# Kernel tuning notes

Hardware: AMD Instinct MI355X
Metric: run time of the kernel (lower is better)

## Reference

```python
import jax, jax.numpy as jnp
import numpy as np

N = 50000          # nodes
E = 1600000        # edges (avg degree 32)
G = 16             # graphs in batch
H = 128            # hidden_dim
HOP = 3
IN_DIM = 1


def setup_inputs() -> dict:
    key = jax.random.key(0)
    ks = jax.random.split(key, 12)
    s = 1.0 / np.sqrt(H)
    return {
        "x": jax.random.normal(ks[0], (N, IN_DIM), jnp.float32),
        "edge_index": jax.random.randint(ks[1], (2, E), 0, N, jnp.int64),
        "edge_attr": jax.random.uniform(ks[2], (E, 1), jnp.float32),
        "batch": jnp.sort(jax.random.randint(ks[3], (N,), 0, G, jnp.int64)),
        "W1": jax.random.normal(ks[4], (HOP, H, IN_DIM), jnp.float32) * s,
        "W2": jax.random.normal(ks[5], (HOP, H, H), jnp.float32) * s,
        "W3": jax.random.normal(ks[6], (HOP, H, H), jnp.float32) * s,
        "W4": jax.random.normal(ks[7], (HOP, H, 1), jnp.float32) * s,
        "W5": jax.random.normal(ks[8], (1, 2 * H), jnp.float32) * s,
        "b5": jnp.zeros((1,), jnp.float32),
        "W6": jax.random.normal(ks[9], (H, H), jnp.float32) * s,
        "W7": jax.random.normal(ks[10], (H, H), jnp.float32) * s,
    }


def reference(x, edge_index, edge_attr, batch, W1, W2, W3, W4, W5, b5, W6, W7):
    row, col = edge_index[0], edge_index[1]
    node_emb = jnp.zeros((N, H), x.dtype)
    for l in range(HOP):
        nfe = x @ W1[l].T                                        # [N,H]
        # gather neighbor embeddings along col, scatter-add to row
        ne_aggr = jax.ops.segment_sum(node_emb[col], row, num_segments=N)
        efe = jax.nn.relu(edge_attr @ W4[l].T)                   # [E,H]
        ee_aggr = jax.ops.segment_sum(efe, row, num_segments=N)  # [N,H]
        node_emb = jax.nn.relu(nfe + ne_aggr @ W2[l].T + ee_aggr @ W3[l].T)
    pooled = jax.ops.segment_sum(node_emb, batch, num_segments=G)  # [G,H]
    sum_emb = pooled @ W6.T                                        # [G,H]
    cat = jax.nn.relu(jnp.concatenate([sum_emb[batch], node_emb @ W7.T], axis=-1))
    return cat @ W5.T + b5                                         # [N,1]
```

## Files before the change

### kernel.cpp

```cpp
#include <hip/hip_runtime.h>
#include <hip/hip_bf16.h>

#define N_NODES 50000
#define N_EDGES 1600000
#define NGRAPH  16
#define HID     128

#define RPB   128
#define NB    ((N_NODES + RPB - 1) / RPB)
#define NBLK  256
#define EPB   ((N_EDGES + NBLK - 1) / NBLK)

typedef unsigned int uint32;
typedef unsigned short ushort;
typedef unsigned char uchar;
typedef __attribute__((ext_vector_type(8))) short bf16x8;
typedef __attribute__((ext_vector_type(4))) float f32x4;
typedef __attribute__((ext_vector_type(2))) float f32x2;

__device__ __forceinline__ uint32 bf16r(float f) {
    uint32 b = __float_as_uint(f);
    return (b + 0x7fffu + ((b >> 16) & 1u)) >> 16;
}
__device__ __forceinline__ uint32 pack_bf16(float lo, float hi) {
    return bf16r(lo) | (bf16r(hi) << 16);
}
__device__ __forceinline__ float bf_lo(uint32 u) { return __uint_as_float(u << 16); }
__device__ __forceinline__ float bf_hi(uint32 u) { return __uint_as_float(u & 0xffff0000u); }

__global__ __launch_bounds__(256) void k_init(float* p, int n,
                                              const int* __restrict__ batch,
                                              int* __restrict__ gstart) {
    int i = blockIdx.x * 256 + threadIdx.x;
    if (i < n) p[i] = 0.f;
    if (i <= NGRAPH) {
        int lo = 0, hi = N_NODES;
        while (lo < hi) {
            int mid = (lo + hi) >> 1;
            if (batch[mid] < i) lo = mid + 1; else hi = mid;
        }
        gstart[i] = lo;
    }
}

__global__ __launch_bounds__(1024) void k_p1_hist(const int* __restrict__ row,
                                                  int* __restrict__ blkhist) {
    __shared__ int hist[NB];
    int tid = threadIdx.x, blk = blockIdx.x;
    for (int i = tid; i < NB; i += 1024) hist[i] = 0;
    __syncthreads();
    int s = blk * EPB, e = s + EPB; if (e > N_EDGES) e = N_EDGES;
    for (int i = s + tid; i < e; i += 1024)
        atomicAdd(&hist[row[i] >> 7], 1);
    __syncthreads();
    for (int i = tid; i < NB; i += 1024)
        blkhist[i * NBLK + blk] = hist[i];
}

__global__ __launch_bounds__(NBLK) void k_p2a(int* __restrict__ blkhist,
                                              int* __restrict__ btot) {
    __shared__ int sums[NBLK];
    int t = threadIdx.x, b = blockIdx.x;
    int v = blkhist[b * NBLK + t];
    sums[t] = v;
    __syncthreads();
    for (int d = 1; d < NBLK; d <<= 1) {
        int u = (t >= d) ? sums[t - d] : 0;
        __syncthreads();
        sums[t] += u;
        __syncthreads();
    }
    blkhist[b * NBLK + t] = sums[t] - v;
    if (t == NBLK - 1) btot[b] = sums[t];
}

__global__ __launch_bounds__(512) void k_p2b(const int* __restrict__ btot,
                                             int* __restrict__ bbase) {
    __shared__ int sums[512];
    int t = threadIdx.x;
    int s = (t < NB) ? btot[t] : 0;
    sums[t] = s;
    __syncthreads();
    for (int d = 1; d < 512; d <<= 1) {
        int v = (t >= d) ? sums[t - d] : 0;
        __syncthreads();
        sums[t] += v;
        __syncthreads();
    }
    if (t < NB) {
        bbase[t] = sums[t] - s;
        if (t == NB - 1) bbase[NB] = sums[t];
    }
}

__global__ __launch_bounds__(1024) void k_p3_part(const int* __restrict__ row,
                                                  const int* __restrict__ col,
                                                  const float* __restrict__ ea,
                                                  const int* __restrict__ blkhist,
                                                  const int* __restrict__ bbase,
                                                  int2* __restrict__ pea) {
    __shared__ int cur[NB];
    int tid = threadIdx.x, blk = blockIdx.x;
    for (int i = tid; i < NB; i += 1024)
        cur[i] = bbase[i] + blkhist[i * NBLK + blk];
    __syncthreads();
    int s = blk * EPB, e = s + EPB; if (e > N_EDGES) e = N_EDGES;
    for (int i = s + tid; i < e; i += 1024) {
        int r = row[i], c = col[i];
        float a = ea[i];
        int slot = atomicAdd(&cur[r >> 7], 1);
        pea[slot] = make_int2(((r & (RPB - 1)) << 16) | c, __float_as_int(a));
    }
}

__global__ __launch_bounds__(512) void k_p4a(const int2* __restrict__ pea,
                                             const int* __restrict__ bbase,
                                             const float* __restrict__ x,
                                             int* __restrict__ offs,
                                             float* __restrict__ ea_sum,
                                             float2* __restrict__ pxe) {
    __shared__ int   cnt[RPB];
    __shared__ float eas[RPB];
    __shared__ int   scan_s[RPB];
    int tid = threadIdx.x, b = blockIdx.x;
    if (tid < RPB) { cnt[tid] = 0; eas[tid] = 0.f; }
    __syncthreads();
    int s = bbase[b], e = bbase[b + 1];
    for (int i = s + tid; i < e; i += 512) {
        int2 p = pea[i];
        int lr = ((uint32)p.x) >> 16;
        atomicAdd(&cnt[lr], 1);
        atomicAdd(&eas[lr], __int_as_float(p.y));
    }
    __syncthreads();
    if (tid < RPB) scan_s[tid] = cnt[tid];
    __syncthreads();
    for (int d = 1; d < RPB; d <<= 1) {
        int v = 0;
        if (tid < RPB && tid >= d) v = scan_s[tid - d];
        __syncthreads();
        if (tid < RPB) scan_s[tid] += v;
        __syncthreads();
    }
    int nbase = b * RPB;
    if (tid < RPB) {
        int excl = scan_s[tid] - cnt[tid];
        int n = nbase + tid;
        if (n < N_NODES) {
            offs[n] = s + excl;
            ea_sum[n] = eas[tid];
            pxe[n] = make_float2(x[n], eas[tid]);
        }
    }
    if (b == NB - 1 && tid == 0) offs[N_NODES] = e;
}

__global__ __launch_bounds__(512) void k_p4b(const int2* __restrict__ pea,
                                             const int* __restrict__ bbase,
                                             const int* __restrict__ offs,
                                             const float2* __restrict__ pxe,
                                             int* __restrict__ csr,
                                             float2* __restrict__ pxec) {
    __shared__ int cur[RPB];
    int tid = threadIdx.x, b = blockIdx.x;
    int nbase = b * RPB;
    if (tid < RPB) cur[tid] = (nbase + tid < N_NODES) ? offs[nbase + tid] : 0;
    __syncthreads();
    int s = bbase[b], e = bbase[b + 1];
    for (int i = s + tid; i < e; i += 512) {
        int2 p = pea[i];
        int c = p.x & 0xFFFF;
        int slot = atomicAdd(&cur[((uint32)p.x) >> 16], 1);
        csr[slot] = c;
        pxec[slot] = pxe[c];
    }
}

__global__ __launch_bounds__(256) void k_prep(const float* __restrict__ W2,
                                              const float* __restrict__ W7,
                                              const float* __restrict__ W3,
                                              const float* __restrict__ W4,
                                              ushort* __restrict__ wpack,
                                              float* __restrict__ v3) {
    int idx = blockIdx.x * 256 + threadIdx.x;
    if (idx < 4 * 16384) {
        int m = idx >> 14, f = idx & 16383;
        int j = f & 7, lane = (f >> 3) & 63, kk = (f >> 9) & 3, t = (f >> 11) & 7;
        int hp = t * 16 + (lane & 15);
        int k  = kk * 32 + ((lane >> 4) & 3) * 8 + j;
        const float* src = (m < 3) ? (W2 + m * HID * HID) : W7;
        wpack[idx] = (ushort)bf16r(src[hp * HID + k]);
    }
    if (idx < 3 * HID) {
        int l = idx / HID, hp = idx % HID;
        float acc = 0.f;
        for (int h = 0; h < HID; h++)
            acc += W3[l * HID * HID + hp * HID + h] * fmaxf(W4[l * HID + h], 0.f);
        v3[idx] = acc;
    }
}

__global__ __launch_bounds__(256) void k_gather1(const float2* __restrict__ pxec,
                                                 const int* __restrict__ offs,
                                                 const float* __restrict__ w1,
                                                 const float* __restrict__ v3,
                                                 uint32* __restrict__ agg) {
    int node = (blockIdx.x * 256 + threadIdx.x) >> 6;
    int lane = threadIdx.x & 63;
    if (node >= N_NODES) return;
    f32x2 w1v = {w1[2 * lane], w1[2 * lane + 1]};
    f32x2 v3v = {v3[2 * lane], v3[2 * lane + 1]};
    const f32x2 zero = {0.f, 0.f};
    int s = offs[node], e = offs[node + 1];
    f32x2 acc[4] = {zero, zero, zero, zero};
    int j = s;
    for (; j + 8 <= e; j += 8) {
        float2 p[8];
#pragma unroll
        for (int u = 0; u < 8; u++) p[u] = pxec[j + u];
#pragma unroll
        for (int u = 0; u < 8; u++) {
            f32x2 px = {p[u].x, p[u].x};
            f32x2 pe = {p[u].y, p[u].y};
            f32x2 r = __builtin_elementwise_fma(px, w1v, pe * v3v);
            acc[u & 3] += __builtin_elementwise_max(r, zero);
        }
    }
    for (; j < e; j++) {
        float2 p = pxec[j];
        f32x2 px = {p.x, p.x};
        f32x2 pe = {p.y, p.y};
        f32x2 r = __builtin_elementwise_fma(px, w1v, pe * v3v);
        acc[0] += __builtin_elementwise_max(r, zero);
    }
    f32x2 rs = (acc[0] + acc[1]) + (acc[2] + acc[3]);
    agg[(size_t)node * 64 + lane] = pack_bf16(rs.x, rs.y);
}

__global__ __launch_bounds__(256) void k_gather(const uchar* __restrict__ emb8,
                                                const int* __restrict__ offs,
                                                const int* __restrict__ csr,
                                                uint32* __restrict__ agg) {
    int node = (blockIdx.x * 256 + threadIdx.x) >> 6;
    int lane = threadIdx.x & 63;
    if (node >= N_NODES) return;
    int s = offs[node], e = offs[node + 1];
    float ax[8] = {0.f}, ay[8] = {0.f};
    for (int base = s; base < e; base += 64) {
        int idx = base + lane;
        int cv = (idx < e) ? csr[idx] : 0;
        int cnt = e - base; if (cnt > 64) cnt = 64;
        int j = 0;
        for (; j + 8 <= cnt; j += 8) {
            int h16[8];
#pragma unroll
            for (int u = 0; u < 8; u++) {
                int c = __shfl(cv, j + u);
                h16[u] = *(const ushort*)(emb8 + (size_t)c * 128 + 2 * lane);
            }
#pragma unroll
            for (int u = 0; u < 8; u++) {
                f32x2 d = __builtin_amdgcn_cvt_pk_f32_fp8(h16[u], false);
                ax[u] += d.x; ay[u] += d.y;
            }
        }
        for (; j < cnt; j++) {
            int c = __shfl(cv, j);
            int h = *(const ushort*)(emb8 + (size_t)c * 128 + 2 * lane);
            f32x2 d = __builtin_amdgcn_cvt_pk_f32_fp8(h, false);
            ax[0] += d.x; ay[0] += d.y;
        }
    }
    float rx = (((ax[0] + ax[1]) + (ax[2] + ax[3])) + ((ax[4] + ax[5]) + (ax[6] + ax[7]))) * 64.f;
    float ry = (((ay[0] + ay[1]) + (ay[2] + ay[3])) + ((ay[4] + ay[5]) + (ay[6] + ay[7]))) * 64.f;
    agg[(size_t)node * 64 + lane] = pack_bf16(rx, ry);
}

#define LROW 136

template <bool LAST>
__global__ __launch_bounds__(256) void k_gemm(const uint32* __restrict__ agg,
                                              const ushort* __restrict__ w2p,
                                              const float* __restrict__ w1l,
                                              const float* __restrict__ v3l,
                                              const float* __restrict__ x,
                                              const float* __restrict__ ea_sum,
                                              uint32* __restrict__ embOut,
                                              uchar* __restrict__ emb8Out,
                                              const ushort* __restrict__ w7p,
                                              const float* __restrict__ W5,
                                              float* __restrict__ outp) {
    __shared__ ushort tile[64 * LROW];
    int tid = threadIdx.x;
    int tbase = blockIdx.x * 64;
    {
        const uint2* src = (const uint2*)(agg + (size_t)tbase * 64);
        int vn = N_NODES - tbase; if (vn > 64) vn = 64;
        int lim = vn * 32;
        for (int i = tid; i < 64 * 32; i += 256) {
            uint2 u = (i < lim) ? src[i] : make_uint2(0u, 0u);
            int r = i >> 5, c4 = (i & 31) * 4;
            *(uint2*)&tile[r * LROW + c4] = u;
        }
    }
    __syncthreads();
    int wv = tid >> 6, lane = tid & 63;
    int n0 = lane & 15, quad = lane >> 4;
    int arow = wv * 16 + n0;
    bf16x8 a0 = *(const bf16x8*)&tile[arow * LROW + 0 * 32 + quad * 8];
    bf16x8 a1 = *(const bf16x8*)&tile[arow * LROW + 1 * 32 + quad * 8];
    bf16x8 a2 = *(const bf16x8*)&tile[arow * LROW + 2 * 32 + quad * 8];
    bf16x8 a3 = *(const bf16x8*)&tile[arow * LROW + 3 * 32 + quad * 8];
    const bf16x8* wb = (const bf16x8*)w2p;
    f32x4 acc[8];
#pragma unroll
    for (int t = 0; t < 8; t++) {
        f32x4 c = {0.f, 0.f, 0.f, 0.f};
        c = __builtin_amdgcn_mfma_f32_16x16x32_bf16(a0, wb[(t * 4 + 0) * 64 + lane], c, 0, 0, 0);
        c = __builtin_amdgcn_mfma_f32_16x16x32_bf16(a1, wb[(t * 4 + 1) * 64 + lane], c, 0, 0, 0);
        c = __builtin_amdgcn_mfma_f32_16x16x32_bf16(a2, wb[(t * 4 + 2) * 64 + lane], c, 0, 0, 0);
        c = __builtin_amdgcn_mfma_f32_16x16x32_bf16(a3, wb[(t * 4 + 3) * 64 + lane], c, 0, 0, 0);
        acc[t] = c;
    }
    float xs[4], es[4];
#pragma unroll
    for (int r = 0; r < 4; r++) {
        int n = tbase + wv * 16 + quad * 4 + r;
        xs[r] = (n < N_NODES) ? x[n] : 0.f;
        es[r] = (n < N_NODES) ? ea_sum[n] : 0.f;
    }
    if (!LAST) {
        uchar* stile = (uchar*)tile;
#pragma unroll
        for (int t = 0; t < 8; t++) {
            int hp = t * 16 + n0;
            float w1v = w1l[hp], v3v = v3l[hp];
#pragma unroll
            for (int r = 0; r < 4; r++) {
                float v = fmaxf(acc[t][r] + xs[r] * w1v + es[r] * v3v, 0.f) * 0.015625f;
                int enc = __builtin_amdgcn_cvt_pk_fp8_f32(v, v, 0, false);
                stile[(wv * 16 + quad * 4 + r) * 136 + hp] = (uchar)(enc & 0xff);
            }
        }
        __syncthreads();
        int vn = N_NODES - tbase; if (vn > 64) vn = 64;
        for (int i = tid; i < 64 * 32; i += 256) {
            int r = i >> 5, c4 = (i & 31) * 4;
            if (r < vn) {
                uint32 u = *(const uint32*)&stile[r * 136 + c4];
                *(uint32*)(emb8Out + (size_t)(tbase + r) * 128 + c4) = u;
            }
        }
    } else {
#pragma unroll
        for (int t = 0; t < 8; t++) {
            int hp = t * 16 + n0;
            float w1v = w1l[hp], v3v = v3l[hp];
#pragma unroll
            for (int r = 0; r < 4; r++) {
                float v = fmaxf(acc[t][r] + xs[r] * w1v + es[r] * v3v, 0.f);
                tile[(wv * 16 + quad * 4 + r) * LROW + hp] = (ushort)bf16r(v);
            }
        }
        __syncthreads();
        {
            int vn = N_NODES - tbase; if (vn > 64) vn = 64;
            for (int i = tid; i < 64 * 32; i += 256) {
                int r = i >> 5, c4 = (i & 31) * 4;
                if (r < vn) {
                    uint2 u = *(const uint2*)&tile[r * LROW + c4];
                    *(uint2*)(embOut + (size_t)(tbase + r) * 64 + (size_t)(i & 31) * 2) = u;
                }
            }
        }
        bf16x8 b0 = *(const bf16x8*)&tile[arow * LROW + 0 * 32 + quad * 8];
        bf16x8 b1 = *(const bf16x8*)&tile[arow * LROW + 1 * 32 + quad * 8];
        bf16x8 b2 = *(const bf16x8*)&tile[arow * LROW + 2 * 32 + quad * 8];
        bf16x8 b3 = *(const bf16x8*)&tile[arow * LROW + 3 * 32 + quad * 8];
        const bf16x8* w7 = (const bf16x8*)w7p;
        float p[4] = {0.f, 0.f, 0.f, 0.f};
#pragma unroll
        for (int t = 0; t < 8; t++) {
            f32x4 c = {0.f, 0.f, 0.f, 0.f};
            c = __builtin_amdgcn_mfma_f32_16x16x32_bf16(b0, w7[(t * 4 + 0) * 64 + lane], c, 0, 0, 0);
            c = __builtin_amdgcn_mfma_f32_16x16x32_bf16(b1, w7[(t * 4 + 1) * 64 + lane], c, 0, 0, 0);
            c = __builtin_amdgcn_mfma_f32_16x16x32_bf16(b2, w7[(t * 4 + 2) * 64 + lane], c, 0, 0, 0);
            c = __builtin_amdgcn_mfma_f32_16x16x32_bf16(b3, w7[(t * 4 + 3) * 64 + lane], c, 0, 0, 0);
            float w5v = W5[128 + t * 16 + n0];
#pragma unroll
            for (int r = 0; r < 4; r++) p[r] += fmaxf(c[r], 0.f) * w5v;
        }
#pragma unroll
        for (int r = 0; r < 4; r++) {
            float v = p[r];
            v += __shfl_xor(v, 1);
            v += __shfl_xor(v, 2);
            v += __shfl_xor(v, 4);
            v += __shfl_xor(v, 8);
            int n = tbase + wv * 16 + quad * 4 + r;
            if (n0 == 0 && n < N_NODES) outp[n] = v;
        }
    }
}

__global__ __launch_bounds__(256) void k_pool2(const uint32* __restrict__ emb,
                                               const int* __restrict__ gstart,
                                               float* __restrict__ pooled) {
    __shared__ float2 red[4][64];
    int bid = blockIdx.x;
    int g = bid >> 4, chunk = bid & 15;
    int gs = gstart[g], ge = gstart[g + 1];
    int len = ge - gs;
    int cs = gs + (int)(((long long)len * chunk) >> 4);
    int ce = gs + (int)(((long long)len * (chunk + 1)) >> 4);
    int sub = threadIdx.x >> 6, lane = threadIdx.x & 63;
    float ax = 0.f, ay = 0.f;
    for (int n = cs + sub; n < ce; n += 4) {
        uint32 u = emb[(size_t)n * 64 + lane];
        ax += bf_lo(u); ay += bf_hi(u);
    }
    red[sub][lane] = make_float2(ax, ay);
    __syncthreads();
    if (sub == 0) {
        float2 r0 = red[0][lane], r1 = red[1][lane], r2 = red[2][lane], r3 = red[3][lane];
        atomicAdd(&pooled[g * HID + 2 * lane],     (r0.x + r1.x) + (r2.x + r3.x));
        atomicAdd(&pooled[g * HID + 2 * lane + 1], (r0.y + r1.y) + (r2.y + r3.y));
    }
}

__global__ __launch_bounds__(128) void k_graph(const float* __restrict__ pooled,
                                               const float* __restrict__ W6,
                                               const float* __restrict__ W5,
                                               float* __restrict__ s_g) {
    int g = blockIdx.x, hp = threadIdx.x;
    float acc = 0.f;
    for (int h = 0; h < HID; h++) acc += pooled[g * HID + h] * W6[hp * HID + h];
    float v = fmaxf(acc, 0.f) * W5[hp];
    __shared__ float red[HID];
    red[hp] = v;
    __syncthreads();
    for (int d = 64; d > 0; d >>= 1) {
        if (hp < d) red[hp] += red[hp + d];
        __syncthreads();
    }
    if (hp == 0) s_g[g] = red[0];
}

__global__ __launch_bounds__(256) void k_addsg(float* __restrict__ out,
                                               const int* __restrict__ batch,
                                               const float* __restrict__ s_g,
                                               const float* __restrict__ b5) {
    int n = blockIdx.x * 256 + threadIdx.x;
    if (n < N_NODES) out[n] += s_g[batch[n]] + b5[0];
}

extern "C" void kernel_launch(void* const* d_in, const int* in_sizes, int n_in,
                              void* d_out, int out_size, void* d_ws, size_t ws_size,
                              hipStream_t stream) {
    (void)in_sizes; (void)n_in; (void)out_size; (void)ws_size;
    const float* x    = (const float*)d_in[0];
    const int*   ei   = (const int*)d_in[1];
    const float* ea   = (const float*)d_in[2];
    const int*   bat  = (const int*)d_in[3];
    const float* W1   = (const float*)d_in[4];
    const float* W2   = (const float*)d_in[5];
    const float* W3   = (const float*)d_in[6];
    const float* W4   = (const float*)d_in[7];
    const float* W5   = (const float*)d_in[8];
    const float* b5   = (const float*)d_in[9];
    const float* W6   = (const float*)d_in[10];
    const float* W7   = (const float*)d_in[11];
    float* out = (float*)d_out;

    const int* row = ei;
    const int* col = ei + N_EDGES;

    float* wsf = (float*)d_ws;
    int*   wsi = (int*)d_ws;
    size_t o = 0;
    float* pooled = wsf + o; o += NGRAPH * HID;
    float* s_g    = wsf + o; o += NGRAPH;
    size_t ztot = o;
    int*   offs   = wsi + o; o += N_NODES + 1;
    float* ea_sum = wsf + o; o += N_NODES;
    int*   gstart = wsi + o; o += NGRAPH + 1;
    int*   btot   = wsi + o; o += NB;
    int*   bbase  = wsi + o; o += NB + 1;
    float* v3     = wsf + o; o += 3 * HID;
    int*   blkh   = wsi + o; o += NB * NBLK;
    o = (o + 1) & ~(size_t)1;
    float2* pxe   = (float2*)(wsi + o); o += 2 * (size_t)N_NODES;
    o = (o + 3) & ~(size_t)3;
    ushort* wpack = (ushort*)(wsi + o); o += 4 * 16384 / 2;
    int*    csr   = wsi + o; o += N_EDGES;
    o = (o + 1) & ~(size_t)1;
    int2*   pea   = (int2*)(wsi + o); o += 2 * (size_t)N_EDGES;
    float2* pxec  = (float2*)(wsi + o); o += 2 * (size_t)N_EDGES;
    o = (o + 1) & ~(size_t)1;
    uint32* embA  = (uint32*)(wsi + o); o += (size_t)N_NODES * 64;
    uchar*  emb8  = (uchar*)(wsi + o);  o += (size_t)N_NODES * 32;
    uint32* aggB  = (uint32*)(wsi + o); o += (size_t)N_NODES * 64;

    const ushort* w2p1 = wpack + 1 * 16384;
    const ushort* w2p2 = wpack + 2 * 16384;
    const ushort* w7p  = wpack + 3 * 16384;

    k_init<<<(int)((ztot + 255) / 256), 256, 0, stream>>>((float*)d_ws, (int)ztot, bat, gstart);
    k_p1_hist<<<NBLK, 1024, 0, stream>>>(row, blkh);
    k_p2a<<<NB, NBLK, 0, stream>>>(blkh, btot);
    k_p2b<<<1, 512, 0, stream>>>(btot, bbase);
    k_p3_part<<<NBLK, 1024, 0, stream>>>(row, col, ea, blkh, bbase, pea);
    k_p4a<<<NB, 512, 0, stream>>>(pea, bbase, x, offs, ea_sum, pxe);
    k_p4b<<<NB, 512, 0, stream>>>(pea, bbase, offs, pxe, csr, pxec);
    k_prep<<<(4 * 16384 + 255) / 256, 256, 0, stream>>>(W2, W7, W3, W4, (ushort*)wpack, v3);
    k_gather1<<<(N_NODES * 64 + 255) / 256, 256, 0, stream>>>(pxec, offs, W1, v3, aggB);
    k_gemm<false><<<(N_NODES + 63) / 64, 256, 0, stream>>>(
        aggB, w2p1, W1 + 1 * HID, v3 + 1 * HID, x, ea_sum, nullptr, emb8, nullptr, nullptr, nullptr);
    k_gather<<<(N_NODES * 64 + 255) / 256, 256, 0, stream>>>(emb8, offs, csr, aggB);
    k_gemm<true><<<(N_NODES + 63) / 64, 256, 0, stream>>>(
        aggB, w2p2, W1 + 2 * HID, v3 + 2 * HID, x, ea_sum, embA, nullptr, w7p, W5, out);
    k_pool2<<<NGRAPH * 16, 256, 0, stream>>>(embA, gstart, pooled);
    k_graph<<<NGRAPH, 128, 0, stream>>>(pooled, W6, W5, s_g);
    k_addsg<<<(N_NODES + 255) / 256, 256, 0, stream>>>(out, bat, s_g, b5);
}
```

Before: 283.5 us.

## Split fp8 embeddings into feature planes and fuse small kernels via last-block pattern

The fp8 node embedding is stored as two 64-byte feature planes. The layer-2 gather now runs twice as many blocks, one per plane, with each lane reading a single byte, which shrinks the per-plane working set so it fits better in cache during random neighbour gathers. Weight packing moves into the init kernel. The two scan kernels and the pool/graph kernels are each merged using an atomic done-counter so the last block finishes the work. This removes several launches but adds atomics, threadfence and serial tail work in a single block.

```diff
diff --git a/kernel.cpp b/kernel.cpp
--- a/kernel.cpp
+++ b/kernel.cpp
@@ -10,6 +10,8 @@
 #define NB    ((N_NODES + RPB - 1) / RPB)
 #define NBLK  256
 #define EPB   ((N_EDGES + NBLK - 1) / NBLK)
+#define PLANESZ ((size_t)N_NODES * 64)
+#define GBLK  ((N_NODES * 64) / 256)
 
 typedef unsigned int uint32;
 typedef unsigned short ushort;
@@ -28,18 +30,39 @@
 __device__ __forceinline__ float bf_lo(uint32 u) { return __uint_as_float(u << 16); }
 __device__ __forceinline__ float bf_hi(uint32 u) { return __uint_as_float(u & 0xffff0000u); }
 
-__global__ __launch_bounds__(256) void k_init(float* p, int n,
+__global__ __launch_bounds__(256) void k_init(float* __restrict__ zp, int zn,
                                               const int* __restrict__ batch,
-                                              int* __restrict__ gstart) {
-    int i = blockIdx.x * 256 + threadIdx.x;
-    if (i < n) p[i] = 0.f;
-    if (i <= NGRAPH) {
+                                              int* __restrict__ gstart,
+                                              const float* __restrict__ W2,
+                                              const float* __restrict__ W7,
+                                              const float* __restrict__ W3,
+                                              const float* __restrict__ W4,
+                                              ushort* __restrict__ wpack,
+                                              float* __restrict__ v3) {
+    int idx = blockIdx.x * 256 + threadIdx.x;
+    if (idx < zn) zp[idx] = 0.f;
+    if (idx <= NGRAPH) {
         int lo = 0, hi = N_NODES;
         while (lo < hi) {
             int mid = (lo + hi) >> 1;
-            if (batch[mid] < i) lo = mid + 1; else hi = mid;
-        }
-        gstart[i] = lo;
+            if (batch[mid] < idx) lo = mid + 1; else hi = mid;
+        }
+        gstart[idx] = lo;
+    }
+    if (idx < 4 * 16384) {
+        int m = idx >> 14, f = idx & 16383;
+        int j = f & 7, lane = (f >> 3) & 63, kk = (f >> 9) & 3, t = (f >> 11) & 7;
+        int hp = t * 16 + (lane & 15);
+        int k  = kk * 32 + ((lane >> 4) & 3) * 8 + j;
+        const float* src = (m < 3) ? (W2 + m * HID * HID) : W7;
+        wpack[idx] = (ushort)bf16r(src[hp * HID + k]);
+    }
+    if (idx < 3 * HID) {
+        int l = idx / HID, hp = idx % HID;
+        float acc = 0.f;
+        for (int h = 0; h < HID; h++)
+            acc += W3[l * HID * HID + hp * HID + h] * fmaxf(W4[l * HID + h], 0.f);
+        v3[idx] = acc;
     }
 }
 
@@ -57,9 +80,12 @@
         blkhist[i * NBLK + blk] = hist[i];
 }
 
-__global__ __launch_bounds__(NBLK) void k_p2a(int* __restrict__ blkhist,
-                                              int* __restrict__ btot) {
+__global__ __launch_bounds__(NBLK) void k_p2(int* __restrict__ blkhist,
+                                             int* __restrict__ btot,
+                                             int* __restrict__ bbase,
+                                             int* __restrict__ done) {
     __shared__ int sums[NBLK];
+    __shared__ int lastflag;
     int t = threadIdx.x, b = blockIdx.x;
     int v = blkhist[b * NBLK + t];
     sums[t] = v;
@@ -72,24 +98,29 @@
     }
     blkhist[b * NBLK + t] = sums[t] - v;
     if (t == NBLK - 1) btot[b] = sums[t];
-}
-
-__global__ __launch_bounds__(512) void k_p2b(const int* __restrict__ btot,
-                                             int* __restrict__ bbase) {
-    __shared__ int sums[512];
-    int t = threadIdx.x;
-    int s = (t < NB) ? btot[t] : 0;
-    sums[t] = s;
-    __syncthreads();
-    for (int d = 1; d < 512; d <<= 1) {
-        int v = (t >= d) ? sums[t - d] : 0;
-        __syncthreads();
-        sums[t] += v;
-        __syncthreads();
-    }
-    if (t < NB) {
-        bbase[t] = sums[t] - s;
-        if (t == NB - 1) bbase[NB] = sums[t];
+    if (t == 0) {
+        __threadfence();
+        int old = atomicAdd(done, 1);
+        lastflag = (old == NB - 1);
+    }
+    __syncthreads();
+    if (lastflag) {
+        int i0 = 2 * t, i1 = 2 * t + 1;
+        int v0 = (i0 < NB) ? atomicAdd(&btot[i0], 0) : 0;
+        int v1 = (i1 < NB) ? atomicAdd(&btot[i1], 0) : 0;
+        int sum = v0 + v1;
+        sums[t] = sum;
+        __syncthreads();
+        for (int d = 1; d < NBLK; d <<= 1) {
+            int u = (t >= d) ? sums[t - d] : 0;
+            __syncthreads();
+            sums[t] += u;
+            __syncthreads();
+        }
+        int excl = sums[t] - sum;
+        if (i0 < NB) bbase[i0] = excl;
+        if (i1 < NB) bbase[i1] = excl + v0;
+        if (t == NBLK - 1) bbase[NB] = sums[t];
     }
 }
 
@@ -173,30 +204,6 @@
         int slot = atomicAdd(&cur[((uint32)p.x) >> 16], 1);
         csr[slot] = c;
         pxec[slot] = pxe[c];
-    }
-}
-
-__global__ __launch_bounds__(256) void k_prep(const float* __restrict__ W2,
-                                              const float* __restrict__ W7,
-                                              const float* __restrict__ W3,
-                                              const float* __restrict__ W4,
-                                              ushort* __restrict__ wpack,
-                                              float* __restrict__ v3) {
-    int idx = blockIdx.x * 256 + threadIdx.x;
-    if (idx < 4 * 16384) {
-        int m = idx >> 14, f = idx & 16383;
-        int j = f & 7, lane = (f >> 3) & 63, kk = (f >> 9) & 3, t = (f >> 11) & 7;
-        int hp = t * 16 + (lane & 15);
-        int k  = kk * 32 + ((lane >> 4) & 3) * 8 + j;
-        const float* src = (m < 3) ? (W2 + m * HID * HID) : W7;
-        wpack[idx] = (ushort)bf16r(src[hp * HID + k]);
-    }
-    if (idx < 3 * HID) {
-        int l = idx / HID, hp = idx % HID;
-        float acc = 0.f;
-        for (int h = 0; h < HID; h++)
-            acc += W3[l * HID * HID + hp * HID + h] * fmaxf(W4[l * HID + h], 0.f);
-        v3[idx] = acc;
     }
 }
 
@@ -237,43 +244,45 @@
     agg[(size_t)node * 64 + lane] = pack_bf16(rs.x, rs.y);
 }
 
-__global__ __launch_bounds__(256) void k_gather(const uchar* __restrict__ emb8,
-                                                const int* __restrict__ offs,
-                                                const int* __restrict__ csr,
-                                                uint32* __restrict__ agg) {
-    int node = (blockIdx.x * 256 + threadIdx.x) >> 6;
+__global__ __launch_bounds__(256) void k_gather8(const uchar* __restrict__ emb8,
+                                                 const int* __restrict__ offs,
+                                                 const int* __restrict__ csr,
+                                                 ushort* __restrict__ agg_us) {
+    int plane = (blockIdx.x >= GBLK) ? 1 : 0;
+    int blk = blockIdx.x - plane * GBLK;
+    int node = (blk * 256 + threadIdx.x) >> 6;
     int lane = threadIdx.x & 63;
     if (node >= N_NODES) return;
+    const uchar* base = emb8 + (size_t)plane * PLANESZ;
     int s = offs[node], e = offs[node + 1];
-    float ax[8] = {0.f}, ay[8] = {0.f};
-    for (int base = s; base < e; base += 64) {
-        int idx = base + lane;
+    float a[8] = {0.f};
+    for (int cb = s; cb < e; cb += 64) {
+        int idx = cb + lane;
         int cv = (idx < e) ? csr[idx] : 0;
-        int cnt = e - base; if (cnt > 64) cnt = 64;
+        int cnt = e - cb; if (cnt > 64) cnt = 64;
         int j = 0;
         for (; j + 8 <= cnt; j += 8) {
-            int h16[8];
+            uint32 bt[8];
 #pragma unroll
             for (int u = 0; u < 8; u++) {
                 int c = __shfl(cv, j + u);
-                h16[u] = *(const ushort*)(emb8 + (size_t)c * 128 + 2 * lane);
+                bt[u] = base[(size_t)c * 64 + lane];
             }
 #pragma unroll
             for (int u = 0; u < 8; u++) {
-                f32x2 d = __builtin_amdgcn_cvt_pk_f32_fp8(h16[u], false);
-                ax[u] += d.x; ay[u] += d.y;
+                f32x2 d = __builtin_amdgcn_cvt_pk_f32_fp8((int)bt[u], false);
+                a[u] += d.x;
             }
         }
         for (; j < cnt; j++) {
             int c = __shfl(cv, j);
-            int h = *(const ushort*)(emb8 + (size_t)c * 128 + 2 * lane);
-            f32x2 d = __builtin_amdgcn_cvt_pk_f32_fp8(h, false);
-            ax[0] += d.x; ay[0] += d.y;
-        }
-    }
-    float rx = (((ax[0] + ax[1]) + (ax[2] + ax[3])) + ((ax[4] + ax[5]) + (ax[6] + ax[7]))) * 64.f;
-    float ry = (((ay[0] + ay[1]) + (ay[2] + ay[3])) + ((ay[4] + ay[5]) + (ay[6] + ay[7]))) * 64.f;
-    agg[(size_t)node * 64 + lane] = pack_bf16(rx, ry);
+            uint32 b1 = base[(size_t)c * 64 + lane];
+            f32x2 d = __builtin_amdgcn_cvt_pk_f32_fp8((int)b1, false);
+            a[0] += d.x;
+        }
+    }
+    float r = (((a[0] + a[1]) + (a[2] + a[3])) + ((a[4] + a[5]) + (a[6] + a[7]))) * 64.f;
+    agg_us[(size_t)node * 128 + plane * 64 + lane] = (ushort)bf16r(r);
 }
 
 #define LROW 136
@@ -348,7 +357,9 @@
             int r = i >> 5, c4 = (i & 31) * 4;
             if (r < vn) {
                 uint32 u = *(const uint32*)&stile[r * 136 + c4];
-                *(uint32*)(emb8Out + (size_t)(tbase + r) * 128 + c4) = u;
+                int plane = c4 >> 6;
+                *(uint32*)(emb8Out + (size_t)plane * PLANESZ +
+                           (size_t)(tbase + r) * 64 + (c4 & 63)) = u;
             }
         }
     } else {
@@ -405,8 +416,13 @@
 
 __global__ __launch_bounds__(256) void k_pool2(const uint32* __restrict__ emb,
                                                const int* __restrict__ gstart,
-                                               float* __restrict__ pooled) {
+                                               float* __restrict__ pooled,
+                                               int* __restrict__ done,
+                                               const float* __restrict__ W6,
+                                               const float* __restrict__ W5,
+                                               float* __restrict__ s_g) {
     __shared__ float2 red[4][64];
+    __shared__ int lastflag;
     int bid = blockIdx.x;
     int g = bid >> 4, chunk = bid & 15;
     int gs = gstart[g], ge = gstart[g + 1];
@@ -426,24 +442,42 @@
         atomicAdd(&pooled[g * HID + 2 * lane],     (r0.x + r1.x) + (r2.x + r3.x));
         atomicAdd(&pooled[g * HID + 2 * lane + 1], (r0.y + r1.y) + (r2.y + r3.y));
     }
-}
-
-__global__ __launch_bounds__(128) void k_graph(const float* __restrict__ pooled,
-                                               const float* __restrict__ W6,
-                                               const float* __restrict__ W5,
-                                               float* __restrict__ s_g) {
-    int g = blockIdx.x, hp = threadIdx.x;
-    float acc = 0.f;
-    for (int h = 0; h < HID; h++) acc += pooled[g * HID + h] * W6[hp * HID + h];
-    float v = fmaxf(acc, 0.f) * W5[hp];
-    __shared__ float red[HID];
-    red[hp] = v;
-    __syncthreads();
-    for (int d = 64; d > 0; d >>= 1) {
-        if (hp < d) red[hp] += red[hp + d];
-        __syncthreads();
-    }
-    if (hp == 0) s_g[g] = red[0];
+    if (threadIdx.x == 0) {
+        __threadfence();
+        int old = atomicAdd(done, 1);
+        lastflag = (old == (int)gridDim.x - 1);
+    }
+    __syncthreads();
+    if (lastflag) {
+        __shared__ float pool_s[NGRAPH * HID];
+        __shared__ float red2[NGRAPH * HID];
+        int tid = threadIdx.x;
+        for (int i = tid; i < NGRAPH * HID; i += 256)
+            pool_s[i] = atomicAdd(&pooled[i], 0.f);
+        __syncthreads();
+        if (tid < HID) {
+            int hp = tid;
+            float acc[NGRAPH];
+#pragma unroll
+            for (int gg = 0; gg < NGRAPH; gg++) acc[gg] = 0.f;
+            for (int h = 0; h < HID; h++) {
+                float wv = W6[hp * HID + h];
+#pragma unroll
+                for (int gg = 0; gg < NGRAPH; gg++)
+                    acc[gg] += pool_s[gg * HID + h] * wv;
+            }
+            float w5v = W5[hp];
+#pragma unroll
+            for (int gg = 0; gg < NGRAPH; gg++)
+                red2[gg * HID + hp] = fmaxf(acc[gg], 0.f) * w5v;
+        }
+        __syncthreads();
+        if (tid < NGRAPH) {
+            float s = 0.f;
+            for (int h = 0; h < HID; h++) s += red2[tid * HID + h];
+            s_g[tid] = s;
+        }
+    }
 }
 
 __global__ __launch_bounds__(256) void k_addsg(float* __restrict__ out,
@@ -480,6 +514,8 @@
     size_t o = 0;
     float* pooled = wsf + o; o += NGRAPH * HID;
     float* s_g    = wsf + o; o += NGRAPH;
+    int*   done_p2   = wsi + o; o += 1;
+    int*   done_pool = wsi + o; o += 1;
     size_t ztot = o;
     int*   offs   = wsi + o; o += N_NODES + 1;
     float* ea_sum = wsf + o; o += N_NODES;
@@ -505,21 +541,19 @@
     const ushort* w2p2 = wpack + 2 * 16384;
     const ushort* w7p  = wpack + 3 * 16384;
 
-    k_init<<<(int)((ztot + 255) / 256), 256, 0, stream>>>((float*)d_ws, (int)ztot, bat, gstart);
+    k_init<<<256, 256, 0, stream>>>((float*)d_ws, (int)ztot, bat, gstart,
+                                    W2, W7, W3, W4, (ushort*)wpack, v3);
     k_p1_hist<<<NBLK, 1024, 0, stream>>>(row, blkh);
-    k_p2a<<<NB, NBLK, 0, stream>>>(blkh, btot);
-    k_p2b<<<1, 512, 0, stream>>>(btot, bbase);
+    k_p2<<<NB, NBLK, 0, stream>>>(blkh, btot, bbase, done_p2);
     k_p3_part<<<NBLK, 1024, 0, stream>>>(row, col, ea, blkh, bbase, pea);
     k_p4a<<<NB, 512, 0, stream>>>(pea, bbase, x, offs, ea_sum, pxe);
     k_p4b<<<NB, 512, 0, stream>>>(pea, bbase, offs, pxe, csr, pxec);
-    k_prep<<<(4 * 16384 + 255) / 256, 256, 0, stream>>>(W2, W7, W3, W4, (ushort*)wpack, v3);
     k_gather1<<<(N_NODES * 64 + 255) / 256, 256, 0, stream>>>(pxec, offs, W1, v3, aggB);
     k_gemm<false><<<(N_NODES + 63) / 64, 256, 0, stream>>>(
         aggB, w2p1, W1 + 1 * HID, v3 + 1 * HID, x, ea_sum, nullptr, emb8, nullptr, nullptr, nullptr);
-    k_gather<<<(N_NODES * 64 + 255) / 256, 256, 0, stream>>>(emb8, offs, csr, aggB);
+    k_gather8<<<2 * GBLK, 256, 0, stream>>>(emb8, offs, csr, (ushort*)aggB);
     k_gemm<true><<<(N_NODES + 63) / 64, 256, 0, stream>>>(
         aggB, w2p2, W1 + 2 * HID, v3 + 2 * HID, x, ea_sum, embA, nullptr, w7p, W5, out);
-    k_pool2<<<NGRAPH * 16, 256, 0, stream>>>(embA, gstart, pooled);
-    k_graph<<<NGRAPH, 128, 0, stream>>>(pooled, W6, W5, s_g);
+    k_pool2<<<NGRAPH * 16, 256, 0, stream>>>(embA, gstart, pooled, done_pool, W6, W5, s_g);
     k_addsg<<<(N_NODES + 255) / 256, 256, 0, stream>>>(out, bat, s_g, b5);
 }
```

Result: slower. 317.3 us (+11.9%).
